# Kernel tuning notes

Hardware: AMD Instinct MI355X
Metric: run time of the kernel (lower is better)

## Reference

```python
import jax, jax.numpy as jnp
import numpy as np

H = 256
LOG_STD_MIN, LOG_STD_MAX = -20.0, 2.0


def setup_inputs() -> dict:
    key = jax.random.key(0)
    ks = jax.random.split(key, 12)
    B, T, F, A = 256, 1000, 64, 16
    s_in = 1.0 / np.sqrt(H)
    inp = {
        "observations": jax.random.normal(ks[0], (B, T, F), jnp.float32),
        # LSTM params (PyTorch gate order: i, f, g, o)
        "W_ih": jax.random.uniform(ks[1], (4 * H, F), jnp.float32, -s_in, s_in),
        "W_hh": jax.random.uniform(ks[2], (4 * H, H), jnp.float32, -s_in, s_in),
        "b_ih": jax.random.uniform(ks[3], (4 * H,), jnp.float32, -s_in, s_in),
        "b_hh": jax.random.uniform(ks[4], (4 * H,), jnp.float32, -s_in, s_in),
        # layer2: Linear(256 -> 256)
        "W2": jax.random.uniform(ks[5], (H, H), jnp.float32, -s_in, s_in),
        "b2": jax.random.uniform(ks[6], (H,), jnp.float32, -s_in, s_in),
        # means head: Linear(256 -> A)
        "Wm": jax.random.uniform(ks[7], (A, H), jnp.float32, -s_in, s_in),
        "bm": jax.random.uniform(ks[8], (A,), jnp.float32, -s_in, s_in),
        # log_stds head: Linear(256 -> A)
        "Ws": jax.random.uniform(ks[9], (A, H), jnp.float32, -s_in, s_in),
        "bs": jax.random.uniform(ks[10], (A,), jnp.float32, -s_in, s_in),
    }
    return inp


def _lstm(observations, W_ih, W_hh, b_ih, b_hh):
    B, T, F = observations.shape
    # Precompute the input-to-gate projection for all timesteps: [T, B, 4H]
    xg = jnp.einsum("btf,gf->tbg", observations, W_ih) + (b_ih + b_hh)
    W_hh_T = W_hh.T  # [H, 4H]

    def step(carry, xg_t):
        h, c = carry  # [B, H] each
        gates = xg_t + h @ W_hh_T  # [B, 4H]
        i, f, g, o = jnp.split(gates, 4, axis=-1)
        i = jax.nn.sigmoid(i)
        f = jax.nn.sigmoid(f)
        g = jnp.tanh(g)
        o = jax.nn.sigmoid(o)
        c = f * c + i * g
        h = o * jnp.tanh(c)
        return (h, c), h

    h0 = jnp.zeros((B, H), observations.dtype)
    c0 = jnp.zeros((B, H), observations.dtype)
    _, hs = jax.lax.scan(step, (h0, c0), xg)  # hs: [T, B, H]
    return jnp.transpose(hs, (1, 0, 2))  # [B, T, H]


def reference(observations, W_ih, W_hh, b_ih, b_hh, W2, b2, Wm, bm, Ws, bs):
    x = _lstm(observations, W_ih, W_hh, b_ih, b_hh)  # [B, T, H]
    x = jax.nn.relu(jnp.einsum("bth,oh->bto", x, W2) + b2)  # [B, T, H]
    means = jnp.einsum("bth,ah->bta", x, Wm) + bm  # [B, T, A]
    log_stds = jnp.einsum("bth,ah->bta", x, Ws) + bs  # [B, T, A]
    stds = jnp.exp(jnp.clip(log_stds, LOG_STD_MIN, LOG_STD_MAX))
    return (means, stds)
```

## Files before the change

kernel.cpp:

```cpp
#include <hip/hip_runtime.h>


#define NB 256
#define NT 1000
#define NF 64
#define NH 256
#define NG 1024
#define NA 16
#define NTHREADS 512
#define CHUNK 8
#define NCHUNK (NT / CHUNK)

typedef _Float16 h2 __attribute__((ext_vector_type(2)));
typedef _Float16 h8 __attribute__((ext_vector_type(8)));
typedef float f4 __attribute__((ext_vector_type(4)));

__device__ __forceinline__ float fdot2(h2 a, h2 b, float c) {
  return __builtin_amdgcn_fdot2(a, b, c, false);
}
__device__ __forceinline__ float fexp2(float x) { return __builtin_amdgcn_exp2f(x); }
__device__ __forceinline__ float frcp(float x) { return __builtin_amdgcn_rcpf(x); }
__device__ __forceinline__ float sigmoidf_(float x) {
  return frcp(1.f + fexp2(-1.4426950408889634f * x));
}
__device__ __forceinline__ float tanhfast(float x) {
  float a = fabsf(x);
  float e = fexp2(-2.8853900817779268f * a);
  float r = (1.f - e) * frcp(1.f + e);
  return __builtin_copysignf(r, x);
}
__device__ __forceinline__ float dot8(h8 x, h8 w, float acc) {
  acc = fdot2(__builtin_shufflevector(x, x, 0, 1), __builtin_shufflevector(w, w, 0, 1), acc);
  acc = fdot2(__builtin_shufflevector(x, x, 2, 3), __builtin_shufflevector(w, w, 2, 3), acc);
  acc = fdot2(__builtin_shufflevector(x, x, 4, 5), __builtin_shufflevector(w, w, 4, 5), acc);
  acc = fdot2(__builtin_shufflevector(x, x, 6, 7), __builtin_shufflevector(w, w, 6, 7), acc);
  return acc;
}

__global__ void prep_kernel(const float* __restrict__ Wih, const float* __restrict__ Whh,
                            const float* __restrict__ bih, const float* __restrict__ bhh,
                            const float* __restrict__ W2, const float* __restrict__ Wm,
                            const float* __restrict__ Ws,
                            h2* __restrict__ whh, h2* __restrict__ wih,
                            h2* __restrict__ w2w, h2* __restrict__ wmh,
                            float* __restrict__ bg) {
  int i = blockIdx.x * 256 + threadIdx.x;
  if (i < 1024 * 128) {
    int j = i >> 7, p = i & 127;
    whh[i] = h2{(_Float16)Whh[j * 256 + 2 * p], (_Float16)Whh[j * 256 + 2 * p + 1]};
  }
  if (i < 1024 * 32) {
    int j = i >> 5, p = i & 31;
    wih[i] = h2{(_Float16)Wih[j * 64 + 2 * p], (_Float16)Wih[j * 64 + 2 * p + 1]};
  }
  if (i < 256 * 128) {
    int j = i >> 7, p = i & 127;
    w2w[i] = h2{(_Float16)W2[j * 256 + 2 * p], (_Float16)W2[j * 256 + 2 * p + 1]};
  }
  if (i < 32 * 128) {
    int j = i >> 7, p = i & 127;
    float v0, v1;
    if (j < 16) { v0 = Wm[j * 256 + 2 * p]; v1 = Wm[j * 256 + 2 * p + 1]; }
    else        { v0 = Ws[(j - 16) * 256 + 2 * p]; v1 = Ws[(j - 16) * 256 + 2 * p + 1]; }
    wmh[i] = h2{(_Float16)v0, (_Float16)v1};
  }
  if (i < 1024) bg[i] = bih[i] + bhh[i];
}

__global__ __launch_bounds__(NTHREADS, 2) void actor_kernel(
    const float* __restrict__ obs,
    const h2* __restrict__ whh, const h2* __restrict__ wih,
    const h2* __restrict__ w2w, const h2* __restrict__ wmh,
    const float* __restrict__ bg, const float* __restrict__ b2,
    const float* __restrict__ bm, const float* __restrict__ bs,
    float* __restrict__ out) {
  __shared__ __align__(16) h8 whh_l[8 * 1024];
  __shared__ __align__(16) _Float16 xg_l[CHUNK * NG];
  __shared__ __align__(16) float gbuf[NG];
  __shared__ __align__(16) h2 hbuf[NH / 2];
  __shared__ __align__(16) h2 hch[CHUNK * NH / 2];
  __shared__ __align__(16) h2 xbuf[CHUNK * NF / 2];
  __shared__ __align__(16) h2 x2b[CHUNK * NH / 2];

  const int tid = threadIdx.x;
  const int b = blockIdx.x;
  const int r0 = tid, r1 = tid + NTHREADS;

  h8 wa8[24], wb8[24];
  {
    const volatile h8* vw = (const volatile h8*)whh;
#pragma unroll
    for (int j = 0; j < 24; j++) wa8[j] = vw[r0 * 32 + 8 + j];
#pragma unroll
    for (int j = 0; j < 24; j++) wb8[j] = vw[r1 * 32 + 8 + j];
  }
  {
    const h8* whh8 = (const h8*)whh;
    for (int k = tid; k < 8 * 1024; k += NTHREADS) {
      int p4 = k >> 10, row = k & 1023;
      whh_l[p4 * 1024 + row] = whh8[row * 32 + p4];
    }
  }
  if (tid < NH / 2) hbuf[tid] = h2{(_Float16)0.f, (_Float16)0.f};
  float c_state = 0.f;
  const float biasg0 = bg[r0], biasg1 = bg[r1];
  const float b2v = b2[tid & 255];
  const int oh = tid & 31;
  const float hbv = (oh < NA) ? bm[oh] : bs[oh - NA];
  __syncthreads();

  const float* obs_b = obs + (size_t)b * NT * NF;
  float* out_means = out;
  float* out_stds = out + (size_t)NB * NT * NA;

  for (int ch = 0; ch < NCHUNK; ++ch) {
    const int t0 = ch * CHUNK;

    if (tid < 128) {
      int t = tid >> 4, fq = tid & 15;
      f4 v = *(const f4*)(obs_b + (size_t)(t0 + t) * NF + fq * 4);
      xbuf[t * 32 + fq * 2] = h2{(_Float16)v[0], (_Float16)v[1]};
      xbuf[t * 32 + fq * 2 + 1] = h2{(_Float16)v[2], (_Float16)v[3]};
    }
    __syncthreads();

#pragma unroll
    for (int rr = 0; rr < 2; ++rr) {
      const int row = rr ? r1 : r0;
      const float bias = rr ? biasg1 : biasg0;
      float acc[CHUNK];
#pragma unroll
      for (int t = 0; t < CHUNK; t++) acc[t] = bias;
      const h8* wrow = (const h8*)wih + row * 8;
#pragma unroll
      for (int jh = 0; jh < 2; jh++) {
        h8 w[4];
#pragma unroll
        for (int q = 0; q < 4; q++) w[q] = wrow[jh * 4 + q];
#pragma unroll
        for (int t = 0; t < CHUNK; t++) {
#pragma unroll
          for (int q = 0; q < 4; q++) {
            h8 xv = *(const h8*)&xbuf[t * 32 + jh * 16 + q * 4];
            acc[t] = dot8(xv, w[q], acc[t]);
          }
        }
      }
#pragma unroll
      for (int t = 0; t < CHUNK; t++) xg_l[t * NG + row] = (_Float16)acc[t];
    }
    __syncthreads();

    for (int t = 0; t < CHUNK; t++) {
      float a0a = (float)xg_l[t * NG + r0], a0b = 0.f;
      float a1a = (float)xg_l[t * NG + r1], a1b = 0.f;
#pragma unroll
      for (int p4 = 0; p4 < 8; p4++) {
        h8 hv = *(const h8*)&hbuf[p4 * 4];
        h8 w0 = whh_l[p4 * 1024 + r0];
        h8 w1 = whh_l[p4 * 1024 + r1];
        if (p4 & 1) { a0b = dot8(hv, w0, a0b); a1b = dot8(hv, w1, a1b); }
        else        { a0a = dot8(hv, w0, a0a); a1a = dot8(hv, w1, a1a); }
      }
#pragma unroll
      for (int j = 0; j < 24; j++) {
        h8 hv = *(const h8*)&hbuf[32 + 4 * j];
        if (j & 1) { a0b = dot8(hv, wa8[j], a0b); a1b = dot8(hv, wb8[j], a1b); }
        else       { a0a = dot8(hv, wa8[j], a0a); a1a = dot8(hv, wb8[j], a1a); }
      }
      gbuf[r0] = a0a + a0b;
      gbuf[r1] = a1a + a1b;
      __syncthreads();
      if (tid < NH) {
        float gi = sigmoidf_(gbuf[tid]);
        float gf = sigmoidf_(gbuf[NH + tid]);
        float gg = tanhfast(gbuf[2 * NH + tid]);
        float go = sigmoidf_(gbuf[3 * NH + tid]);
        c_state = gf * c_state + gi * gg;
        float hval = go * tanhfast(c_state);
        _Float16 hh = (_Float16)hval;
        ((_Float16*)hbuf)[tid] = hh;
        ((_Float16*)hch)[t * NH + tid] = hh;
      }
      __syncthreads();
    }

    {
      const int o = tid & 255;
      const int tb = (tid >> 8) * 4;
      float acc[4] = {b2v, b2v, b2v, b2v};
      const h8* wrow = (const h8*)w2w + o * 32;
#pragma unroll 2
      for (int c = 0; c < 8; c++) {
        h8 w[4];
#pragma unroll
        for (int q = 0; q < 4; q++) w[q] = wrow[c * 4 + q];
#pragma unroll
        for (int tt = 0; tt < 4; tt++) {
#pragma unroll
          for (int q = 0; q < 4; q++) {
            h8 xv = *(const h8*)&hch[(tb + tt) * 128 + c * 16 + q * 4];
            acc[tt] = dot8(xv, w[q], acc[tt]);
          }
        }
      }
#pragma unroll
      for (int tt = 0; tt < 4; tt++)
        ((_Float16*)x2b)[(tb + tt) * NH + o] = (_Float16)fmaxf(acc[tt], 0.f);
    }
    __syncthreads();

    if (tid < 256) {
      const int tt = tid >> 5;
      const h8* wrow = (const h8*)wmh + oh * 32;
      float acc = 0.f;
#pragma unroll 4
      for (int c = 0; c < 32; c++) {
        h8 xv = *(const h8*)&x2b[tt * 128 + c * 4];
        acc = dot8(xv, wrow[c], acc);
      }
      acc += hbv;
      const size_t idx = ((size_t)b * NT + (t0 + tt)) * NA + (oh & 15);
      if (oh < NA) {
        out_means[idx] = acc;
      } else {
        float ls = fminf(fmaxf(acc, -20.f), 2.f);
        out_stds[idx] = fexp2(1.4426950408889634f * ls);
      }
    }
  }
}

extern "C" void kernel_launch(void* const* d_in, const int* in_sizes, int n_in,
                              void* d_out, int out_size, void* d_ws, size_t ws_size,
                              hipStream_t stream) {
  const float* obs = (const float*)d_in[0];
  const float* Wih = (const float*)d_in[1];
  const float* Whh = (const float*)d_in[2];
  const float* bih = (const float*)d_in[3];
  const float* bhh = (const float*)d_in[4];
  const float* W2 = (const float*)d_in[5];
  const float* b2 = (const float*)d_in[6];
  const float* Wm = (const float*)d_in[7];
  const float* bm = (const float*)d_in[8];
  const float* Ws = (const float*)d_in[9];
  const float* bs = (const float*)d_in[10];

  char* ws = (char*)d_ws;
  h2* whh = (h2*)(ws + 0);
  h2* wih = (h2*)(ws + 524288);
  h2* w2w = (h2*)(ws + 655360);
  h2* wmh = (h2*)(ws + 786432);
  float* bg = (float*)(ws + 802816);

  prep_kernel<<<512, 256, 0, stream>>>(Wih, Whh, bih, bhh, W2, Wm, Ws,
                                       whh, wih, w2w, wmh, bg);
  actor_kernel<<<NB, NTHREADS, 0, stream>>>(obs, whh, wih, w2w, wmh, bg, b2, bm,
                                            bs, (float*)d_out);
}
```

Before: 4.448 ms.

## Split recurrent matvec by K-halves so each thread computes all four gates

The recurrent step's work is reassigned. Before, each thread computed two full gate rows. Now each thread handles one hidden unit's four gates (i, f, g, o) over half of the hidden dimension. The upper half-block writes its partial sums to a small f4 buffer, and the lower half combines them with the xg input term and applies the activations directly. This drops the 1024-float gate buffer round trip and the scattered reads of four gates from shared memory, at the cost of a partial-sum exchange. Register weights are rearranged to 48 h8 per thread, the same count as before, and the LDS weight layout is permuted to match.

```diff
diff --git a/kernel.cpp b/kernel.cpp
--- a/kernel.cpp
+++ b/kernel.cpp
@@ -76,7 +76,7 @@
     float* __restrict__ out) {
   __shared__ __align__(16) h8 whh_l[8 * 1024];
   __shared__ __align__(16) _Float16 xg_l[CHUNK * NG];
-  __shared__ __align__(16) float gbuf[NG];
+  __shared__ __align__(16) f4 pbuf[NH];
   __shared__ __align__(16) h2 hbuf[NH / 2];
   __shared__ __align__(16) h2 hch[CHUNK * NH / 2];
   __shared__ __align__(16) h2 xbuf[CHUNK * NF / 2];
@@ -84,25 +84,28 @@
 
   const int tid = threadIdx.x;
   const int b = blockIdx.x;
-  const int r0 = tid, r1 = tid + NTHREADS;
-
-  h8 wa8[24], wb8[24];
+  const int half = tid >> 8;
+  const int j = tid & 255;
+
+  h8 wreg[48];
   {
     const volatile h8* vw = (const volatile h8*)whh;
 #pragma unroll
-    for (int j = 0; j < 24; j++) wa8[j] = vw[r0 * 32 + 8 + j];
-#pragma unroll
-    for (int j = 0; j < 24; j++) wb8[j] = vw[r1 * 32 + 8 + j];
+    for (int g = 0; g < 4; g++)
+#pragma unroll
+      for (int m = 0; m < 12; m++)
+        wreg[g * 12 + m] = vw[(g * 256 + j) * 32 + half * 16 + 4 + m];
   }
   {
     const h8* whh8 = (const h8*)whh;
     for (int k = tid; k < 8 * 1024; k += NTHREADS) {
-      int p4 = k >> 10, row = k & 1023;
-      whh_l[p4 * 1024 + row] = whh8[row * 32 + p4];
+      int q = k >> 10, row = k & 1023;
+      whh_l[q * 1024 + row] = whh8[row * 32 + (q >> 2) * 16 + (q & 3)];
     }
   }
   if (tid < NH / 2) hbuf[tid] = h2{(_Float16)0.f, (_Float16)0.f};
   float c_state = 0.f;
+  const int r0 = tid, r1 = tid + NTHREADS;
   const float biasg0 = bg[r0], biasg1 = bg[r1];
   const float b2v = b2[tid & 255];
   const int oh = tid & 31;
@@ -152,35 +155,41 @@
     __syncthreads();
 
     for (int t = 0; t < CHUNK; t++) {
-      float a0a = (float)xg_l[t * NG + r0], a0b = 0.f;
-      float a1a = (float)xg_l[t * NG + r1], a1b = 0.f;
-#pragma unroll
-      for (int p4 = 0; p4 < 8; p4++) {
-        h8 hv = *(const h8*)&hbuf[p4 * 4];
-        h8 w0 = whh_l[p4 * 1024 + r0];
-        h8 w1 = whh_l[p4 * 1024 + r1];
-        if (p4 & 1) { a0b = dot8(hv, w0, a0b); a1b = dot8(hv, w1, a1b); }
-        else        { a0a = dot8(hv, w0, a0a); a1a = dot8(hv, w1, a1a); }
-      }
-#pragma unroll
-      for (int j = 0; j < 24; j++) {
-        h8 hv = *(const h8*)&hbuf[32 + 4 * j];
-        if (j & 1) { a0b = dot8(hv, wa8[j], a0b); a1b = dot8(hv, wb8[j], a1b); }
-        else       { a0a = dot8(hv, wa8[j], a0a); a1a = dot8(hv, wb8[j], a1a); }
-      }
-      gbuf[r0] = a0a + a0b;
-      gbuf[r1] = a1a + a1b;
+      float a0 = 0.f, a1 = 0.f, a2 = 0.f, a3 = 0.f;
+#pragma unroll
+      for (int p4 = 0; p4 < 4; p4++) {
+        h8 hv = *(const h8*)&hbuf[half * 64 + p4 * 4];
+        const h8* wl = &whh_l[(half * 4 + p4) * 1024 + j];
+        a0 = dot8(hv, wl[0], a0);
+        a1 = dot8(hv, wl[256], a1);
+        a2 = dot8(hv, wl[512], a2);
+        a3 = dot8(hv, wl[768], a3);
+      }
+#pragma unroll
+      for (int m = 0; m < 12; m++) {
+        h8 hv = *(const h8*)&hbuf[half * 64 + 16 + 4 * m];
+        a0 = dot8(hv, wreg[m], a0);
+        a1 = dot8(hv, wreg[12 + m], a1);
+        a2 = dot8(hv, wreg[24 + m], a2);
+        a3 = dot8(hv, wreg[36 + m], a3);
+      }
+      if (half) pbuf[j] = f4{a0, a1, a2, a3};
       __syncthreads();
-      if (tid < NH) {
-        float gi = sigmoidf_(gbuf[tid]);
-        float gf = sigmoidf_(gbuf[NH + tid]);
-        float gg = tanhfast(gbuf[2 * NH + tid]);
-        float go = sigmoidf_(gbuf[3 * NH + tid]);
+      if (!half) {
+        f4 o4 = pbuf[j];
+        float gi = a0 + o4.x + (float)xg_l[t * NG + j];
+        float gf = a1 + o4.y + (float)xg_l[t * NG + 256 + j];
+        float gg = a2 + o4.z + (float)xg_l[t * NG + 512 + j];
+        float go = a3 + o4.w + (float)xg_l[t * NG + 768 + j];
+        gi = sigmoidf_(gi);
+        gf = sigmoidf_(gf);
+        gg = tanhfast(gg);
+        go = sigmoidf_(go);
         c_state = gf * c_state + gi * gg;
         float hval = go * tanhfast(c_state);
         _Float16 hh = (_Float16)hval;
-        ((_Float16*)hbuf)[tid] = hh;
-        ((_Float16*)hch)[t * NH + tid] = hh;
+        ((_Float16*)hbuf)[j] = hh;
+        ((_Float16*)hch)[t * NH + j] = hh;
       }
       __syncthreads();
     }
```

After: 4.455 ms. No clear change (+0.2%).
